# Optimization experiments

Measured on AMD Instinct MI355X. Metric: run time of the kernel, lower is better.

The kernel has to match this reference:

```python
import jax, jax.numpy as jnp
import numpy as np

KH, KW = 3, 3
PAD = (1, 1, 1, 1)  # torch F.pad order: (W_left, W_right, H_top, H_bottom)
STRIDE = 1
B, CIN, COUT, H, W = 4, 32, 32, 128, 128


def setup_inputs() -> dict:
    key = jax.random.key(0)
    k1, k2, k3, k4 = jax.random.split(key, 4)
    f = jax.random.normal(k1, (B, CIN, H, W), jnp.float32)
    # orientation field components (cos/sin of a random angle field)
    theta = jax.random.uniform(k2, (B, CIN, H, W), jnp.float32, 0.0, 2.0 * np.pi)
    r0 = jnp.cos(theta)
    r1 = jnp.sin(theta)
    # learned conv weight (nn.Conv2d default uniform init, no bias)
    fan_in = CIN * KH * KW
    bound = 1.0 / np.sqrt(fan_in)
    w = jax.random.uniform(k3, (COUT, CIN, KH, KW), jnp.float32, -bound, bound)
    # frozen wr: (randn * pi * 100) / a with a = 100  ->  randn * pi
    wr = jax.random.normal(k4, (COUT, CIN, KH, KW), jnp.float32) * np.pi
    return {"f": f, "r0": r0, "r1": r1, "w": w, "wr": wr}


def _rot90(w):
    # torch: w.permute(0,1,2,4,3).flip([4]) on the (kh,kw) dims
    return jnp.flip(jnp.swapaxes(w, -1, -2), -1)


def _conv_single(f, r0, r1, w, wr):
    # f, r0, r1: (B, Cin, Hp, Wp);  w, wr: (Cout, Cin, KH, KW)
    Hp, Wp = f.shape[2], f.shape[3]
    he = Hp - PAD[0] - PAD[1]
    we = Wp - PAD[2] - PAD[3]
    s = STRIDE
    out = None
    for i in range(KH):
        for j in range(KW):
            fw = f[:, :, i:i + he:s, j:j + we:s]    # (B, Cin, h, w)
            r0w = r0[:, :, i:i + he:s, j:j + we:s]
            r1w = r1[:, :, i:i + he:s, j:j + we:s]
            c = jnp.cos(wr[:, :, i, j])[None, :, :, None, None]   # (1, Cout, Cin, 1, 1)
            sn = jnp.sin(wr[:, :, i, j])[None, :, :, None, None]
            # lambda_theta: relu of orientation-projected field, (B, Cout, Cin, h, w)
            lam = jax.nn.relu(c * r0w[:, None] + sn * r1w[:, None])
            term = jnp.einsum('bchw,oc,bochw->bohw', fw, w[:, :, i, j], lam)
            out = term if out is None else out + term
    return out  # (B, Cout, h, w)


def _forward(f, r0, r1, w, wr):
    pl, pr, pt, pb = PAD
    pad = ((0, 0), (0, 0), (pt, pb), (pl, pr))
    fp = jnp.pad(f, pad)
    r0p = jnp.pad(r0, pad)
    r1p = jnp.pad(r1, pad)
    orient = jnp.arange(4, dtype=f.dtype) * jnp.asarray(np.pi / 2, f.dtype)
    outs = []
    wk = w
    for o in range(4):
        if o > 0:
            wk = _rot90(wk)
        outs.append(_conv_single(fp, r0p, r1p, wk, wr + orient[o]))
    stacked = jnp.stack(outs, axis=2)              # (B, Cout, 4, h, w)
    idx = jnp.argmax(stacked, axis=2)              # (B, Cout, h, w)
    out = jnp.take_along_axis(stacked, idx[:, :, None], axis=2)[:, :, 0]
    out_r = orient[idx]                            # winning orientation angle
    return out, jnp.cos(out_r), jnp.sin(out_r)


def reference(f, r0, r1, w, wr):
    return _forward(f, r0, r1, w, wr)
```

## Files before the change

### kernel.cpp

```cpp
#include <hip/hip_runtime.h>


#define B_    4
#define CIN_  32
#define COUT_ 32
#define H_    128
#define W_    128
#define HW_   (H_ * W_)
#define OUTSZ_ (B_ * COUT_ * H_ * W_)

__global__ __launch_bounds__(256)
void build_wtab(const float* __restrict__ w, const float* __restrict__ wr,
                float* __restrict__ tab)
{
    int idx = blockIdx.x * 256 + threadIdx.x;
    if (idx >= CIN_ * 9 * COUT_) return;
    int oc  = idx & 31;
    int t2  = idx >> 5;
    int tap = t2 % 9;
    int cc  = t2 / 9;
    int i = tap / 3, j = tap - i * 3;
    int base = (oc * CIN_ + cc) * 9;
    float w0 = w[base + i * 3 + j];
    float w1 = w[base + (2 - j) * 3 + i];
    float w2 = w[base + (2 - i) * 3 + (2 - j)];
    float w3 = w[base + j * 3 + (2 - i)];
    float S, C;
    sincosf(wr[base + i * 3 + j], &S, &C);
    float* dst = tab + (size_t)idx * 8;
    dst[0] = C;  dst[1] = S;
    dst[2] = w0; dst[3] = w1;
    dst[4] = w2; dst[5] = w3;
    dst[6] = 0.0f; dst[7] = 0.0f;
}

#define NC_    4
#define NG_    (CIN_ / NC_)
#define RSTR_  68
#define CLSTR_ (3 * RSTR_)
#define USED_  (NC_ * CLSTR_)
#define ASZ_   (USED_ + 4)

__global__ __launch_bounds__(256)
void orient_conv_kernel(const float* __restrict__ f,
                        const float* __restrict__ r0,
                        const float* __restrict__ r1,
                        const float* __restrict__ tab,
                        float* __restrict__ out)
{
    __shared__ float sF[ASZ_], sR0[ASZ_], sR1[ASZ_];

    const int tid   = threadIdx.x;
    const int oc    = tid & 31;
    const int pxg   = tid >> 5;
    const int px0   = pxg << 3;
    const int bid   = blockIdx.x;
    const int b     = bid >> 8;
    const int rem   = bid & 255;
    const int h     = rem >> 1;
    const int wbase = (rem & 1) << 6;

    int      goff[4], sidx[4];
    unsigned msk[4];
#pragma unroll
    for (int k = 0; k < 4; ++k) {
        int s = tid + (k << 8);
        if (s < USED_) {
            int cl  = s / CLSTR_;
            int r2  = s - cl * CLSTR_;
            int row = r2 / RSTR_;
            int col = r2 - row * RSTR_;
            int gh = h + row - 1;
            int gw = wbase + col - 1;
            bool ok = (col < 66) & ((unsigned)gh < (unsigned)H_) &
                      ((unsigned)gw < (unsigned)W_);
            goff[k] = ok ? (cl * HW_ + gh * W_ + gw) : 0;
            msk[k]  = ok ? 0xFFFFFFFFu : 0u;
            sidx[k] = s;
        } else { goff[k] = 0; msk[k] = 0u; sidx[k] = USED_; }
    }
    const bool have3 = (tid + 768) < USED_;
    const int chanBase = b * (CIN_ * HW_);

    float acc[8][4];
#pragma unroll
    for (int p = 0; p < 8; ++p)
#pragma unroll
        for (int o = 0; o < 4; ++o) acc[p][o] = 0.0f;

    float tF[4], tA[4], tB[4];
    {
        const float* fb = f  + chanBase;
        const float* ab = r0 + chanBase;
        const float* bb = r1 + chanBase;
#pragma unroll
        for (int k = 0; k < 3; ++k) {
            tF[k] = fb[goff[k]]; tA[k] = ab[goff[k]]; tB[k] = bb[goff[k]];
        }
        if (have3) { tF[3] = fb[goff[3]]; tA[3] = ab[goff[3]]; tB[3] = bb[goff[3]]; }
    }

#pragma unroll 1
    for (int g = 0; g < NG_; ++g) {
        __syncthreads();
#pragma unroll
        for (int k = 0; k < 3; ++k) {
            sF [sidx[k]] = __uint_as_float(__float_as_uint(tF[k]) & msk[k]);
            sR0[sidx[k]] = __uint_as_float(__float_as_uint(tA[k]) & msk[k]);
            sR1[sidx[k]] = __uint_as_float(__float_as_uint(tB[k]) & msk[k]);
        }
        if (have3) {
            sF [sidx[3]] = __uint_as_float(__float_as_uint(tF[3]) & msk[3]);
            sR0[sidx[3]] = __uint_as_float(__float_as_uint(tA[3]) & msk[3]);
            sR1[sidx[3]] = __uint_as_float(__float_as_uint(tB[3]) & msk[3]);
        }
        __syncthreads();

        if (g + 1 < NG_) {
            const int gb = chanBase + (g + 1) * (NC_ * HW_);
            const float* fb = f  + gb;
            const float* ab = r0 + gb;
            const float* bb = r1 + gb;
#pragma unroll
            for (int k = 0; k < 3; ++k) {
                tF[k] = fb[goff[k]]; tA[k] = ab[goff[k]]; tB[k] = bb[goff[k]];
            }
            if (have3) { tF[3] = fb[goff[3]]; tA[3] = ab[goff[3]]; tB[3] = bb[goff[3]]; }
        }

#pragma unroll 1
        for (int cl = 0; cl < NC_; ++cl) {
            const int cc = g * NC_ + cl;
            const float* wb0 = tab + (size_t)(((cc * 9 + 2) << 5) | oc) * 8;
            const float* wb1 = wb0 + 4 * 256;
#pragma unroll
            for (int i = 0; i < 3; ++i) {
                const int bi = cl * CLSTR_ + i * RSTR_ + px0;
                float4 Fa = *reinterpret_cast<const float4*>(&sF [bi]);
                float4 Fb = *reinterpret_cast<const float4*>(&sF [bi + 4]);
                float2 Fc = *reinterpret_cast<const float2*>(&sF [bi + 8]);
                float4 Aa = *reinterpret_cast<const float4*>(&sR0[bi]);
                float4 Ab = *reinterpret_cast<const float4*>(&sR0[bi + 4]);
                float2 Ac = *reinterpret_cast<const float2*>(&sR0[bi + 8]);
                float4 Ba = *reinterpret_cast<const float4*>(&sR1[bi]);
                float4 Bb = *reinterpret_cast<const float4*>(&sR1[bi + 4]);
                float2 Bc = *reinterpret_cast<const float2*>(&sR1[bi + 8]);
                const float fin[10]  = {Fa.x, Fa.y, Fa.z, Fa.w, Fb.x, Fb.y,
                                        Fb.z, Fb.w, Fc.x, Fc.y};
                const float ain[10]  = {Aa.x, Aa.y, Aa.z, Aa.w, Ab.x, Ab.y,
                                        Ab.z, Ab.w, Ac.x, Ac.y};
                const float bin_[10] = {Ba.x, Ba.y, Ba.z, Ba.w, Bb.x, Bb.y,
                                        Bb.z, Bb.w, Bc.x, Bc.y};
#pragma unroll
                for (int j = 0; j < 3; ++j) {
                    const int tap = i * 3 + j;
                    const float* wp = (tap < 5) ? (wb0 + (tap - 2) * 256)
                                                : (wb1 + (tap - 6) * 256);
                    float4 W4 = *reinterpret_cast<const float4*>(wp);
                    float2 W2 = *reinterpret_cast<const float2*>(wp + 4);
                    const float C  = W4.x, S  = W4.y;
                    const float w0 = W4.z, w1 = W4.w;
                    const float w2 = W2.x, w3 = W2.y;
#pragma unroll
                    for (int p = 0; p < 8; ++p) {
                        const float fv  = fin [p + j];
                        const float r0v = ain [p + j];
                        const float r1v = bin_[p + j];
                        float u  = fmaf(C, r0v, S * r1v);
                        float vv = fmaf(C, r1v, -(S * r0v));
                        float g0 = fmaxf(u,  0.0f);
                        float g1 = fmaxf(vv, 0.0f);
                        float g2 = g0 - u;
                        float g3 = g1 - vv;
                        acc[p][0] = fmaf(fv * g0, w0, acc[p][0]);
                        acc[p][1] = fmaf(fv * g1, w1, acc[p][1]);
                        acc[p][2] = fmaf(fv * g2, w2, acc[p][2]);
                        acc[p][3] = fmaf(fv * g3, w3, acc[p][3]);
                    }
                }
            }
        }
    }

    const float cosv[4] = {1.0f, -4.37113883e-08f, -1.0f, 1.19248806e-08f};
    const float sinv[4] = {0.0f, 1.0f, -8.74227766e-08f, -1.0f};
#pragma unroll
    for (int p = 0; p < 8; ++p) {
        int wcol = wbase + px0 + p;
        float a0 = acc[p][0], a1 = acc[p][1];
        float a2 = acc[p][2], a3 = acc[p][3];
        float best = a0; int bi = 0;
        if (a1 > best) { best = a1; bi = 1; }
        if (a2 > best) { best = a2; bi = 2; }
        if (a3 > best) { best = a3; bi = 3; }
        size_t o = ((size_t)(b * COUT_ + oc) * H_ + h) * W_ + wcol;
        out[o]              = best;
        out[o + OUTSZ_]     = cosv[bi];
        out[o + 2 * OUTSZ_] = sinv[bi];
    }
}

extern "C" void kernel_launch(void* const* d_in, const int* in_sizes, int n_in,
                              void* d_out, int out_size, void* d_ws, size_t ws_size,
                              hipStream_t stream)
{
    const float* f  = (const float*)d_in[0];
    const float* r0 = (const float*)d_in[1];
    const float* r1 = (const float*)d_in[2];
    const float* w  = (const float*)d_in[3];
    const float* wr = (const float*)d_in[4];
    float* out = (float*)d_out;
    float* tab = (float*)d_ws;

    build_wtab<<<dim3(36), dim3(256), 0, stream>>>(w, wr, tab);
    orient_conv_kernel<<<dim3(B_ * H_ * 2), dim3(256), 0, stream>>>(
        f, r0, r1, tab, out);
}
```

Before: 298.6 us.

## Vectorize orientation conv with packed float2 math and interleaved smem layout

Recasts the inner loop to use two-wide float vectors so the compiler can emit packed FP32 FMA/mul instructions, pairing columns 32 apart through an interleaved shared-memory layout. The block grows to 512 threads, each handling 4 pixels instead of 8, and each channel group stages 8 input channels instead of 4. It also folds the negative-part terms into fused multiply-adds. The aim is higher ALU throughput and more threads per block, at the cost of more weight-table loads per output and different register pressure.

```diff
diff --git a/kernel.cpp b/kernel.cpp
--- a/kernel.cpp
+++ b/kernel.cpp
@@ -1,5 +1,7 @@
 #include <hip/hip_runtime.h>
 
+
+typedef float v2f __attribute__((ext_vector_type(2)));
 
 #define B_    4
 #define CIN_  32
@@ -34,26 +36,26 @@
     dst[6] = 0.0f; dst[7] = 0.0f;
 }
 
-#define NC_    4
+#define NC_    8
 #define NG_    (CIN_ / NC_)
-#define RSTR_  68
-#define CLSTR_ (3 * RSTR_)
+#define ROWF_  68
+#define CLSTR_ (3 * ROWF_)
 #define USED_  (NC_ * CLSTR_)
-#define ASZ_   (USED_ + 4)
-
-__global__ __launch_bounds__(256)
+#define PLANE_ 1636
+
+__global__ __launch_bounds__(512, 4)
 void orient_conv_kernel(const float* __restrict__ f,
                         const float* __restrict__ r0,
                         const float* __restrict__ r1,
                         const float* __restrict__ tab,
                         float* __restrict__ out)
 {
-    __shared__ float sF[ASZ_], sR0[ASZ_], sR1[ASZ_];
+    __shared__ float sm[3 * PLANE_];
 
     const int tid   = threadIdx.x;
     const int oc    = tid & 31;
     const int pxg   = tid >> 5;
-    const int px0   = pxg << 3;
+    const int p     = pxg << 1;
     const int bid   = blockIdx.x;
     const int b     = bid >> 8;
     const int rem   = bid & 255;
@@ -64,29 +66,29 @@
     unsigned msk[4];
 #pragma unroll
     for (int k = 0; k < 4; ++k) {
-        int s = tid + (k << 8);
+        int s = tid + (k << 9);
         if (s < USED_) {
             int cl  = s / CLSTR_;
             int r2  = s - cl * CLSTR_;
-            int row = r2 / RSTR_;
-            int col = r2 - row * RSTR_;
+            int row = r2 / ROWF_;
+            int q2  = r2 - row * ROWF_;
+            int col = (q2 >> 1) + ((q2 & 1) << 5);
             int gh = h + row - 1;
             int gw = wbase + col - 1;
-            bool ok = (col < 66) & ((unsigned)gh < (unsigned)H_) &
-                      ((unsigned)gw < (unsigned)W_);
+            bool ok = ((unsigned)gh < (unsigned)H_) & ((unsigned)gw < (unsigned)W_);
             goff[k] = ok ? (cl * HW_ + gh * W_ + gw) : 0;
             msk[k]  = ok ? 0xFFFFFFFFu : 0u;
             sidx[k] = s;
         } else { goff[k] = 0; msk[k] = 0u; sidx[k] = USED_; }
     }
-    const bool have3 = (tid + 768) < USED_;
+    const bool have3 = (tid + 1536) < USED_;
     const int chanBase = b * (CIN_ * HW_);
 
-    float acc[8][4];
-#pragma unroll
-    for (int p = 0; p < 8; ++p)
-#pragma unroll
-        for (int o = 0; o < 4; ++o) acc[p][o] = 0.0f;
+    v2f acc[2][4];
+#pragma unroll
+    for (int q = 0; q < 2; ++q)
+#pragma unroll
+        for (int o = 0; o < 4; ++o) acc[q][o] = (v2f)(0.0f);
 
     float tF[4], tA[4], tB[4];
     {
@@ -105,14 +107,14 @@
         __syncthreads();
 #pragma unroll
         for (int k = 0; k < 3; ++k) {
-            sF [sidx[k]] = __uint_as_float(__float_as_uint(tF[k]) & msk[k]);
-            sR0[sidx[k]] = __uint_as_float(__float_as_uint(tA[k]) & msk[k]);
-            sR1[sidx[k]] = __uint_as_float(__float_as_uint(tB[k]) & msk[k]);
+            sm[             sidx[k]] = __uint_as_float(__float_as_uint(tF[k]) & msk[k]);
+            sm[PLANE_     + sidx[k]] = __uint_as_float(__float_as_uint(tA[k]) & msk[k]);
+            sm[2 * PLANE_ + sidx[k]] = __uint_as_float(__float_as_uint(tB[k]) & msk[k]);
         }
         if (have3) {
-            sF [sidx[3]] = __uint_as_float(__float_as_uint(tF[3]) & msk[3]);
-            sR0[sidx[3]] = __uint_as_float(__float_as_uint(tA[3]) & msk[3]);
-            sR1[sidx[3]] = __uint_as_float(__float_as_uint(tB[3]) & msk[3]);
+            sm[             sidx[3]] = __uint_as_float(__float_as_uint(tF[3]) & msk[3]);
+            sm[PLANE_     + sidx[3]] = __uint_as_float(__float_as_uint(tA[3]) & msk[3]);
+            sm[2 * PLANE_ + sidx[3]] = __uint_as_float(__float_as_uint(tB[3]) & msk[3]);
         }
         __syncthreads();
 
@@ -135,22 +137,16 @@
             const float* wb1 = wb0 + 4 * 256;
 #pragma unroll
             for (int i = 0; i < 3; ++i) {
-                const int bi = cl * CLSTR_ + i * RSTR_ + px0;
-                float4 Fa = *reinterpret_cast<const float4*>(&sF [bi]);
-                float4 Fb = *reinterpret_cast<const float4*>(&sF [bi + 4]);
-                float2 Fc = *reinterpret_cast<const float2*>(&sF [bi + 8]);
-                float4 Aa = *reinterpret_cast<const float4*>(&sR0[bi]);
-                float4 Ab = *reinterpret_cast<const float4*>(&sR0[bi + 4]);
-                float2 Ac = *reinterpret_cast<const float2*>(&sR0[bi + 8]);
-                float4 Ba = *reinterpret_cast<const float4*>(&sR1[bi]);
-                float4 Bb = *reinterpret_cast<const float4*>(&sR1[bi + 4]);
-                float2 Bc = *reinterpret_cast<const float2*>(&sR1[bi + 8]);
-                const float fin[10]  = {Fa.x, Fa.y, Fa.z, Fa.w, Fb.x, Fb.y,
-                                        Fb.z, Fb.w, Fc.x, Fc.y};
-                const float ain[10]  = {Aa.x, Aa.y, Aa.z, Aa.w, Ab.x, Ab.y,
-                                        Ab.z, Ab.w, Ac.x, Ac.y};
-                const float bin_[10] = {Ba.x, Ba.y, Ba.z, Ba.w, Bb.x, Bb.y,
-                                        Bb.z, Bb.w, Bc.x, Bc.y};
+                const int bi = cl * CLSTR_ + i * ROWF_ + (p << 1);
+                float4 fA = *reinterpret_cast<const float4*>(&sm[bi]);
+                float4 fB = *reinterpret_cast<const float4*>(&sm[bi + 4]);
+                float4 aA = *reinterpret_cast<const float4*>(&sm[PLANE_ + bi]);
+                float4 aB = *reinterpret_cast<const float4*>(&sm[PLANE_ + bi + 4]);
+                float4 bA = *reinterpret_cast<const float4*>(&sm[2 * PLANE_ + bi]);
+                float4 bB = *reinterpret_cast<const float4*>(&sm[2 * PLANE_ + bi + 4]);
+                v2f fP[4]  = {{fA.x, fA.y}, {fA.z, fA.w}, {fB.x, fB.y}, {fB.z, fB.w}};
+                v2f aP[4]  = {{aA.x, aA.y}, {aA.z, aA.w}, {aB.x, aB.y}, {aB.z, aB.w}};
+                v2f bP[4]  = {{bA.x, bA.y}, {bA.z, bA.w}, {bB.x, bB.y}, {bB.z, bB.w}};
 #pragma unroll
                 for (int j = 0; j < 3; ++j) {
                     const int tap = i * 3 + j;
@@ -158,24 +154,31 @@
                                                 : (wb1 + (tap - 6) * 256);
                     float4 W4 = *reinterpret_cast<const float4*>(wp);
                     float2 W2 = *reinterpret_cast<const float2*>(wp + 4);
-                    const float C  = W4.x, S  = W4.y;
-                    const float w0 = W4.z, w1 = W4.w;
-                    const float w2 = W2.x, w3 = W2.y;
-#pragma unroll
-                    for (int p = 0; p < 8; ++p) {
-                        const float fv  = fin [p + j];
-                        const float r0v = ain [p + j];
-                        const float r1v = bin_[p + j];
-                        float u  = fmaf(C, r0v, S * r1v);
-                        float vv = fmaf(C, r1v, -(S * r0v));
-                        float g0 = fmaxf(u,  0.0f);
-                        float g1 = fmaxf(vv, 0.0f);
-                        float g2 = g0 - u;
-                        float g3 = g1 - vv;
-                        acc[p][0] = fmaf(fv * g0, w0, acc[p][0]);
-                        acc[p][1] = fmaf(fv * g1, w1, acc[p][1]);
-                        acc[p][2] = fmaf(fv * g2, w2, acc[p][2]);
-                        acc[p][3] = fmaf(fv * g3, w3, acc[p][3]);
+                    v2f C2  = {W4.x, W4.x};
+                    v2f S2  = {W4.y, W4.y};
+                    v2f w02 = {W4.z, W4.z};
+                    v2f w12 = {W4.w, W4.w};
+                    v2f w22 = {W2.x, W2.x};
+                    v2f w32 = {W2.y, W2.y};
+#pragma unroll
+                    for (int q = 0; q < 2; ++q) {
+                        v2f fv  = fP[q + j];
+                        v2f r0v = aP[q + j];
+                        v2f r1v = bP[q + j];
+                        v2f m1 = S2 * r1v;
+                        v2f u  = __builtin_elementwise_fma(C2, r0v, m1);
+                        v2f m2 = S2 * r0v;
+                        v2f vv = __builtin_elementwise_fma(C2, r1v, -m2);
+                        v2f g0 = __builtin_elementwise_max(u,  (v2f)(0.0f));
+                        v2f g1 = __builtin_elementwise_max(vv, (v2f)(0.0f));
+                        v2f t0 = fv * g0;
+                        v2f t1 = fv * g1;
+                        v2f t2 = __builtin_elementwise_fma(fv, -u,  t0);
+                        v2f t3 = __builtin_elementwise_fma(fv, -vv, t1);
+                        acc[q][0] = __builtin_elementwise_fma(t0, w02, acc[q][0]);
+                        acc[q][1] = __builtin_elementwise_fma(t1, w12, acc[q][1]);
+                        acc[q][2] = __builtin_elementwise_fma(t2, w22, acc[q][2]);
+                        acc[q][3] = __builtin_elementwise_fma(t3, w32, acc[q][3]);
                     }
                 }
             }
@@ -185,18 +188,21 @@
     const float cosv[4] = {1.0f, -4.37113883e-08f, -1.0f, 1.19248806e-08f};
     const float sinv[4] = {0.0f, 1.0f, -8.74227766e-08f, -1.0f};
 #pragma unroll
-    for (int p = 0; p < 8; ++p) {
-        int wcol = wbase + px0 + p;
-        float a0 = acc[p][0], a1 = acc[p][1];
-        float a2 = acc[p][2], a3 = acc[p][3];
-        float best = a0; int bi = 0;
-        if (a1 > best) { best = a1; bi = 1; }
-        if (a2 > best) { best = a2; bi = 2; }
-        if (a3 > best) { best = a3; bi = 3; }
-        size_t o = ((size_t)(b * COUT_ + oc) * H_ + h) * W_ + wcol;
-        out[o]              = best;
-        out[o + OUTSZ_]     = cosv[bi];
-        out[o + 2 * OUTSZ_] = sinv[bi];
+    for (int q = 0; q < 2; ++q) {
+#pragma unroll
+        for (int k = 0; k < 2; ++k) {
+            int wcol = wbase + p + q + (k << 5);
+            float a0 = acc[q][0][k], a1 = acc[q][1][k];
+            float a2 = acc[q][2][k], a3 = acc[q][3][k];
+            float best = a0; int bi = 0;
+            if (a1 > best) { best = a1; bi = 1; }
+            if (a2 > best) { best = a2; bi = 2; }
+            if (a3 > best) { best = a3; bi = 3; }
+            size_t o = ((size_t)(b * COUT_ + oc) * H_ + h) * W_ + wcol;
+            out[o]              = best;
+            out[o + OUTSZ_]     = cosv[bi];
+            out[o + 2 * OUTSZ_] = sinv[bi];
+        }
     }
 }
 
@@ -213,6 +219,6 @@
     float* tab = (float*)d_ws;
 
     build_wtab<<<dim3(36), dim3(256), 0, stream>>>(w, wr, tab);
-    orient_conv_kernel<<<dim3(B_ * H_ * 2), dim3(256), 0, stream>>>(
+    orient_conv_kernel<<<dim3(B_ * H_ * 2), dim3(512), 0, stream>>>(
         f, r0, r1, tab, out);
 }
```

Measured after the change: 288.7 us. 1.03x faster.
